# Performance work log

Measured on AMD Instinct MI355X. Metric: run time of the kernel, lower is better.

## Reference

```python
import jax, jax.numpy as jnp
import numpy as np

B, T, D, H, L = 2, 1000, 768, 12, 2
DK = D // H
MLP_HID = D * 1  # mlp_ratio = 1
WIDTHS = [7, 15, 31, 63, 127, 255, 7, 15, 31, 63, 127, 255]


def _band_mask():
    # diagonal_mask(seq_len, mask_width): True = blocked (outside the diagonal band)
    i = np.arange(T)[:, None]
    j = np.arange(T)[None, :]
    m = np.stack([np.abs(i - j) > (w // 2) for w in WIDTHS], 0)  # (H, T, T)
    return jnp.asarray(m)


def _rel_pos_emb():
    # espnet-style RelPositionalEncoding: rel positions T-1 .. -(T-1), shape (2T-1, D)
    pos = jnp.arange(T - 1, -T, -1, dtype=jnp.float32)
    div = jnp.exp(jnp.arange(0, D, 2, dtype=jnp.float32) * (-np.log(10000.0) / D))
    ang = pos[:, None] * div[None, :]
    return jnp.stack([jnp.sin(ang), jnp.cos(ang)], -1).reshape(2 * T - 1, D)


def setup_inputs() -> dict:
    key = jax.random.key(0)
    ks = iter(jax.random.split(key, 32))
    rn = lambda sh, s=0.02: jax.random.normal(next(ks), sh, jnp.float32) * s
    return {
        "x": jax.random.normal(next(ks), (B, T, D), jnp.float32),
        "mask": _band_mask(),
        "ln1_g": jnp.ones((L, D)), "ln1_b": jnp.zeros((L, D)),
        "wq": rn((L, D, D)), "bq": jnp.zeros((L, D)),
        "wk": rn((L, D, D)), "bk": jnp.zeros((L, D)),
        "wv": rn((L, D, D)), "bv": jnp.zeros((L, D)),
        "wo": rn((L, D, D)), "bo": jnp.zeros((L, D)),
        "wpos": rn((L, D, D)),
        "pbu": rn((L, H, DK)), "pbv": rn((L, H, DK)),
        "ln2_g": jnp.ones((L, D)), "ln2_b": jnp.zeros((L, D)),
        "w1": rn((L, D, MLP_HID)), "b1": jnp.zeros((L, MLP_HID)),
        "w2": rn((L, MLP_HID, D)), "b2": jnp.zeros((L, D)),
    }


def _ln(x, g, b):
    m = jnp.mean(x, -1, keepdims=True)
    v = jnp.var(x, -1, keepdims=True)
    return (x - m) * jax.lax.rsqrt(v + 1e-5) * g + b


def _rel_shift(x):
    # x: (b, h, t, 2t-1) -> shifted so column s corresponds to rel pos (t-1 - s + row offset)
    b, h, t, n = x.shape
    x = jnp.pad(x, ((0, 0), (0, 0), (0, 0), (1, 0)))        # (b,h,t,2t)
    x = x.reshape(b, h, n + 1, t)[:, :, 1:, :].reshape(b, h, t, n)
    return x[..., :t]


def _forward(x, mask, p):
    (ln1_g, ln1_b, wq, bq, wk, bk, wv, bv, wo, bo,
     wpos, pbu, pbv, ln2_g, ln2_b, w1, b1, w2, b2) = p
    pe = _rel_pos_emb()                                      # (2T-1, D)
    x = x * jnp.asarray(np.sqrt(D), x.dtype)                 # xscale in RelPositionalEncoding
    neg = jnp.asarray(-1e30, x.dtype)
    inv_sqrt_dk = 1.0 / np.sqrt(DK)
    for l in range(L):
        h = _ln(x, ln1_g[l], ln1_b[l])
        q = (h @ wq[l] + bq[l]).reshape(B, T, H, DK)
        k = (h @ wk[l] + bk[l]).reshape(B, T, H, DK)
        v = (h @ wv[l] + bv[l]).reshape(B, T, H, DK)
        pp = (pe @ wpos[l]).reshape(2 * T - 1, H, DK)        # pos projection (no bias)
        ac = jnp.einsum('bthd,bshd->bhts', q + pbu[l], k)    # content term
        bd = _rel_shift(jnp.einsum('bthd,nhd->bhtn', q + pbv[l], pp))  # position term
        s = (ac + bd) * inv_sqrt_dk
        s = jnp.where(mask[None], neg, s)                    # per-head diagonal band mask
        a = jax.nn.softmax(s, axis=-1)
        o = jnp.einsum('bhts,bshd->bthd', a, v).reshape(B, T, D) @ wo[l] + bo[l]
        x = x + o
        h2 = _ln(x, ln2_g[l], ln2_b[l])
        x = x + (jax.nn.gelu(h2 @ w1[l] + b1[l], approximate=False) @ w2[l] + b2[l])
    return x


def reference(x, mask, ln1_g, ln1_b, wq, bq, wk, bk, wv, bv, wo, bo, wpos, pbu, pbv, ln2_g, ln2_b, w1, b1, w2, b2):
    return _forward(x, mask, (ln1_g, ln1_b, wq, bq, wk, bk, wv, bv, wo, bo,
                              wpos, pbu, pbv, ln2_g, ln2_b, w1, b1, w2, b2))
```

## Files before the change

### kernel.cpp

```cpp
#include <hip/hip_runtime.h>

#define TT 1000
#define BB 2
#define DD 768
#define HH 12
#define DK 64
#define LL 2
#define WELEM 589824
#define PEROWS 255
#define VTP 1312
#define PPL 195840

typedef __bf16 bf16x8 __attribute__((ext_vector_type(8)));
typedef float floatx4 __attribute__((ext_vector_type(4)));

__device__ __constant__ int HALFW[12] = {3,7,15,31,63,127,3,7,15,31,63,127};
__device__ __constant__ int HORD[12]  = {5,11,4,10,3,9,2,8,1,7,0,6};

__device__ __forceinline__ float b2f(unsigned short u){
    union { unsigned int i; float f; } x; x.i = ((unsigned int)u) << 16; return x.f;
}
__device__ __forceinline__ unsigned short f2b(float f){
    union { float f; unsigned int i; } x; x.f = f;
    unsigned int i = x.i;
    i += 0x7fffu + ((i >> 16) & 1u);
    return (unsigned short)(i >> 16);
}
__device__ __forceinline__ void gload16(const void* g, void* l){
    __builtin_amdgcn_global_load_lds(
        (const __attribute__((address_space(1))) void*)g,
        (__attribute__((address_space(3))) void*)l, 16, 0, 0);
}

__global__ __launch_bounds__(256)
void prep_kernel(const float* s0, const float* s1, const float* s2, const float* s3,
                 const float* s4, const float* s5, const float* s6,
                 unsigned short* __restrict__ dst,
                 const float* __restrict__ x, float* __restrict__ xc,
                 unsigned short* __restrict__ pe){
    int z = blockIdx.z;
    int tid = threadIdx.x;
    if (z < 14){
        const float* srcs[7] = {s0,s1,s2,s3,s4,s5,s6};
        const float* src = srcs[z % 7] + (size_t)(z / 7)*WELEM;
        unsigned short* d = dst + (size_t)z*WELEM;
        int k0 = blockIdx.x*64, n0 = blockIdx.y*64;
        __shared__ __align__(16) unsigned short tile[64][72];
        int r = tid >> 2, c = tid & 3;
        const float4* sp = (const float4*)(src + (size_t)(k0+r)*DD + n0 + c*16);
        float4 f0 = sp[0], f1 = sp[1], f2 = sp[2], f3 = sp[3];
        unsigned short u[16];
        u[0]=f2b(f0.x); u[1]=f2b(f0.y); u[2]=f2b(f0.z); u[3]=f2b(f0.w);
        u[4]=f2b(f1.x); u[5]=f2b(f1.y); u[6]=f2b(f1.z); u[7]=f2b(f1.w);
        u[8]=f2b(f2.x); u[9]=f2b(f2.y); u[10]=f2b(f2.z); u[11]=f2b(f2.w);
        u[12]=f2b(f3.x); u[13]=f2b(f3.y); u[14]=f2b(f3.z); u[15]=f2b(f3.w);
        *(int4*)&tile[r][c*16]   = *(int4*)&u[0];
        *(int4*)&tile[r][c*16+8] = *(int4*)&u[8];
        __syncthreads();
        unsigned short tmp[16];
        #pragma unroll
        for (int i=0;i<16;++i) tmp[i] = tile[c*16+i][r];
        int4* dp = (int4*)(d + (size_t)(n0+r)*DD + k0 + c*16);
        dp[0] = *(int4*)&tmp[0];
        dp[1] = *(int4*)&tmp[8];
    } else if (z == 14){
        int id = blockIdx.y*12 + blockIdx.x;
        for (int i = id*256 + tid; i < 384000; i += 36864){
            float4 v = ((const float4*)x)[i];
            v.x *= 27.712812921102035f; v.y *= 27.712812921102035f;
            v.z *= 27.712812921102035f; v.w *= 27.712812921102035f;
            ((float4*)xc)[i] = v;
        }
    } else {
        int bid = blockIdx.y*12 + blockIdx.x;
        #pragma unroll
        for (int rr = 0; rr < 2; ++rr){
            int row = bid*2 + rr;
            if (row < PEROWS){
                float pos = (float)(127 - row);
                int i = tid;
                float dv = expf((float)(2*i) * (-9.210340371976184f / 768.0f));
                float ang = pos * dv;
                pe[(size_t)row*DD + 2*i]   = f2b(sinf(ang));
                pe[(size_t)row*DD + 2*i+1] = f2b(cosf(ang));
                if (tid < 128){
                    int j = 256 + tid;
                    float dv2 = expf((float)(2*j) * (-9.210340371976184f / 768.0f));
                    float an2 = pos * dv2;
                    pe[(size_t)row*DD + 2*j]   = f2b(sinf(an2));
                    pe[(size_t)row*DD + 2*j+1] = f2b(cosf(an2));
                }
            }
        }
    }
}

__global__ __launch_bounds__(256)
void ln_kernel(const float* __restrict__ x, const float* __restrict__ g,
               const float* __restrict__ bb, unsigned short* __restrict__ out){
    int row = blockIdx.x;
    const float* xr = x + (size_t)row*DD;
    int tid = threadIdx.x;
    float v0 = xr[tid], v1 = xr[tid+256], v2 = xr[tid+512];
    float s = v0+v1+v2, ss = v0*v0+v1*v1+v2*v2;
    #pragma unroll
    for (int o=1;o<64;o<<=1){ s += __shfl_xor(s,o); ss += __shfl_xor(ss,o); }
    __shared__ float rs[4], rss[4];
    int wv = tid>>6, lane = tid&63;
    if (lane==0){ rs[wv]=s; rss[wv]=ss; }
    __syncthreads();
    s  = rs[0]+rs[1]+rs[2]+rs[3];
    ss = rss[0]+rss[1]+rss[2]+rss[3];
    float mean = s * (1.0f/768.0f);
    float var  = ss * (1.0f/768.0f) - mean*mean;
    float inv  = 1.0f / sqrtf(var + 1e-5f);
    unsigned short* orow = out + (size_t)row*DD;
    #pragma unroll
    for (int kk=0;kk<3;++kk){
        int i = tid + 256*kk;
        float v = (kk==0?v0:(kk==1?v1:v2));
        orow[i] = f2b((v - mean)*inv*g[i] + bb[i]);
    }
}

#define GEMM_GL64(A_, Bt_, n0_, M_)                                             \
    int tid = threadIdx.x;                                                      \
    int m0 = blockIdx.x*64;                                                     \
    int wv = tid>>6, lane = tid&63;                                             \
    int quad = lane>>4, l16 = lane&15;                                          \
    floatx4 acc[4];                                                             \
    _Pragma("unroll")                                                           \
    for (int ni=0;ni<4;++ni) acc[ni] = (floatx4){0.f,0.f,0.f,0.f};              \
    {                                                                           \
      int rl0 = wv*16 + (lane>>3);                                              \
      int rl1 = rl0 + 8;                                                        \
      int gc  = (lane&7) ^ (lane>>3);                                           \
      int ra0 = m0 + rl0; if (ra0 > (M_)-1) ra0 = (M_)-1;                       \
      int ra1 = m0 + rl1; if (ra1 > (M_)-1) ra1 = (M_)-1;                       \
      const char* gA0 = (const char*)(A_)  + (size_t)ra0*1536 + gc*16;          \
      const char* gA1 = (const char*)(A_)  + (size_t)ra1*1536 + gc*16;          \
      const char* gB0 = (const char*)(Bt_) + (size_t)((n0_)+rl0)*1536 + gc*16;  \
      const char* gB1 = (const char*)(Bt_) + (size_t)((n0_)+rl1)*1536 + gc*16;  \
      char* shB = (char*)sh;                                                    \
      int ld0 = (2*wv)*1024, ld1 = (2*wv+1)*1024;                               \
      int arow = (16*wv + l16)*64;                                              \
      int sw8  = l16 & 7;                                                       \
      int cq0 = (quad ^ sw8)*8;                                                 \
      int cq1 = ((4|quad) ^ sw8)*8;                                             \
      gload16(gA0, shB + ld0);                                                  \
      gload16(gA1, shB + ld1);                                                  \
      gload16(gB0, shB + 8192 + ld0);                                           \
      gload16(gB1, shB + 8192 + ld1);                                           \
      for (int s=0; s<12; ++s){                                                 \
        if (s < 11){                                                            \
          char* nb = shB + ((s+1)&1)*16384;                                     \
          int off = (s+1)*128;                                                  \
          gload16(gA0 + off, nb + ld0);                                         \
          gload16(gA1 + off, nb + ld1);                                         \
          gload16(gB0 + off, nb + 8192 + ld0);                                  \
          gload16(gB1 + off, nb + 8192 + ld1);                                  \
          asm volatile("s_waitcnt vmcnt(4)" ::: "memory");                      \
        } else {                                                                \
          asm volatile("s_waitcnt vmcnt(0)" ::: "memory");                      \
        }                                                                       \
        __builtin_amdgcn_s_barrier();                                           \
        __builtin_amdgcn_sched_barrier(0);                                      \
        const unsigned short* cA = sh + (s&1)*8192;                             \
        const unsigned short* cB = cA + 4096;                                   \
        _Pragma("unroll")                                                       \
        for (int kh=0; kh<2; ++kh){                                             \
          int cq = kh ? cq1 : cq0;                                              \
          bf16x8 af = *(const bf16x8*)&cA[arow + cq];                           \
          _Pragma("unroll")                                                     \
          for (int ni=0; ni<4; ++ni){                                           \
            bf16x8 bfv = *(const bf16x8*)&cB[ni*1024 + l16*64 + cq];            \
            acc[ni] = __builtin_amdgcn_mfma_f32_16x16x32_bf16(af, bfv, acc[ni], 0,0,0); \
          }                                                                     \
        }                                                                       \
        __builtin_amdgcn_sched_barrier(0);                                      \
        __builtin_amdgcn_s_barrier();                                           \
      }                                                                         \
    }

template<int MODE>
__global__ __launch_bounds__(256)
void gemm_kernel(const unsigned short* __restrict__ A, const unsigned short* __restrict__ Bt,
                 const float* __restrict__ bias, unsigned short* __restrict__ outb,
                 float* __restrict__ resid, int M){
    __shared__ __align__(16) unsigned short sh[16384];
    int n0 = blockIdx.y*64;
    GEMM_GL64(A, Bt, n0, M)
    float bfv_[4];
    #pragma unroll
    for (int ni=0;ni<4;++ni) bfv_[ni] = bias ? bias[n0 + 16*ni + l16] : 0.0f;
    #pragma unroll
    for (int rr=0;rr<4;++rr){
        int row = m0 + 16*wv + 4*quad + rr;
        if (row >= M) continue;
        #pragma unroll
        for (int ni=0;ni<4;++ni){
            int col = n0 + 16*ni + l16;
            float v = acc[ni][rr] + bfv_[ni];
            if (MODE == 1)      outb[(size_t)row*768 + col] = f2b(0.5f*v*(1.0f + erff(v*0.70710678118654752f)));
            else                resid[(size_t)row*768 + col] += v;
        }
    }
}

__global__ __launch_bounds__(256)
void gemm_pos_kernel(const unsigned short* __restrict__ A, const unsigned short* __restrict__ Bt,
                     unsigned short* __restrict__ outb){
    __shared__ __align__(16) unsigned short sh[16384];
    int n0 = blockIdx.y*64;
    int zz = blockIdx.z;
    const unsigned short* Bt_ = Bt + (size_t)zz*7*WELEM;
    unsigned short* outb_ = outb + (size_t)zz*PPL;
    GEMM_GL64(A, Bt_, n0, PEROWS)
    #pragma unroll
    for (int rr=0;rr<4;++rr){
        int row = m0 + 16*wv + 4*quad + rr;
        if (row >= PEROWS) continue;
        #pragma unroll
        for (int ni=0;ni<4;++ni){
            int col = n0 + 16*ni + l16;
            int h = col >> 6, d = col & 63;
            outb_[((size_t)h*PEROWS + row)*DK + d] = f2b(acc[ni][rr]);
        }
    }
}

__global__ __launch_bounds__(256)
void gemm_qkv_kernel(const unsigned short* __restrict__ A, const unsigned short* __restrict__ Bt,
                     const float* __restrict__ bq, const float* __restrict__ bk, const float* __restrict__ bv,
                     unsigned short* __restrict__ qout, unsigned short* __restrict__ kout,
                     unsigned short* __restrict__ vout){
    __shared__ __align__(16) unsigned short sh[16384];
    int n0 = blockIdx.y*64;
    GEMM_GL64(A, Bt, n0, 2000)
    int sec = blockIdx.y / 12;
    int col0 = n0 - sec*768;
    int h = col0 >> 6;
    const float* bias = (sec==0) ? bq : (sec==1) ? bk : bv;
    float bfv_[4];
    #pragma unroll
    for (int ni=0;ni<4;++ni) bfv_[ni] = bias[col0 + 16*ni + l16];
    if (sec != 2){
        unsigned short* outp = (sec==0) ? qout : kout;
        #pragma unroll
        for (int rr=0;rr<4;++rr){
            int row = m0 + 16*wv + 4*quad + rr;
            if (row >= 2000) continue;
            int b = row / TT, tl = row - b*TT;
            #pragma unroll
            for (int ni=0;ni<4;++ni){
                int d = 16*ni + l16;
                outp[(((size_t)(b*HH + h))*TT + tl)*DK + d] = f2b(acc[ni][rr] + bfv_[ni]);
            }
        }
    } else {
        #pragma unroll
        for (int rr=0;rr<4;++rr){
            int rt = 16*wv + 4*quad + rr;
            #pragma unroll
            for (int ni=0;ni<4;++ni)
                sh[rt*66 + 16*ni + l16] = f2b(acc[ni][rr] + bfv_[ni]);
        }
        __syncthreads();
        #pragma unroll
        for (int it=0; it<16; ++it){
            int idx = it*256 + tid;
            int d = idx >> 6, rt = idx & 63;
            int row = m0 + rt;
            if (row < 2000){
                int b = row / TT, tl = row - b*TT;
                vout[(((size_t)(b*HH + h))*DK + d)*VTP + tl + 128] = sh[rt*66 + d];
            }
        }
    }
}

__global__ __launch_bounds__(256)
void attn_kernel(const unsigned short* __restrict__ q, const unsigned short* __restrict__ k,
                 const unsigned short* __restrict__ vT, const unsigned short* __restrict__ pp,
                 const float* __restrict__ pbu, const float* __restrict__ pbv,
                 unsigned short* __restrict__ out){
    int b = blockIdx.y, h = HORD[blockIdx.z];
    int t0 = blockIdx.x * 16;
    int w2 = HALFW[h];
    int tid = threadIdx.x;
    int wv = tid >> 6, lane = tid & 63;
    int l16 = lane & 15, quad = lane >> 4;

    const unsigned short* qB = q  + ((size_t)(b*HH + h))*TT*DK;
    const unsigned short* kB = k  + ((size_t)(b*HH + h))*TT*DK;
    const unsigned short* vB = vT + ((size_t)(b*HH + h))*DK*VTP;
    const unsigned short* pB = pp + (size_t)h*PEROWS*DK;

    __shared__ __align__(16) float bd[16*260];
    __shared__ __align__(16) unsigned short pl[16*328];
    __shared__ float sms[4][16];

    int tq = t0 + l16; if (tq > TT-1) tq = TT-1;
    union { int4 i; unsigned short u[8]; } r0, r1;
    r0.i = *(const int4*)(qB + (size_t)tq*DK + quad*8);
    r1.i = *(const int4*)(qB + (size_t)tq*DK + 32 + quad*8);
    const float* pu = pbu + h*DK + quad*8;
    const float* pv = pbv + h*DK + quad*8;
    union { unsigned short u[8]; bf16x8 v; } qu0, qu1, qv0, qv1;
    #pragma unroll
    for (int i=0;i<8;++i){
        float a0 = b2f(r0.u[i]), a1 = b2f(r1.u[i]);
        qu0.u[i] = f2b(a0 + pu[i]);
        qu1.u[i] = f2b(a1 + pu[32+i]);
        qv0.u[i] = f2b(a0 + pv[i]);
        qv1.u[i] = f2b(a1 + pv[32+i]);
    }

    int Nn = 2*w2 + 1;
    int ntiles = (Nn + 15) >> 4;
    for (int ti = wv; ti < ntiles; ti += 4){
        int n = 127 - w2 + ti*16 + l16; if (n > PEROWS-1) n = PEROWS-1;
        const unsigned short* pr = pB + (size_t)n*DK + quad*8;
        bf16x8 pb0 = *(const bf16x8*)pr;
        bf16x8 pb1 = *(const bf16x8*)(pr + 32);
        floatx4 a = {0.f,0.f,0.f,0.f};
        a = __builtin_amdgcn_mfma_f32_16x16x32_bf16(qv0.v, pb0, a, 0,0,0);
        a = __builtin_amdgcn_mfma_f32_16x16x32_bf16(qv1.v, pb1, a, 0,0,0);
        #pragma unroll
        for (int r=0;r<4;++r) bd[(quad*4+r)*260 + ti*16 + l16] = a[r];
    }
    for (int i = tid; i < 16*328/4; i += 256)
        ((unsigned long long*)pl)[i] = 0ULL;
    __syncthreads();

    int Ns = 2*w2 + 16;
    int stiles = (Ns + 15) >> 4;
    int s_lo = t0 - w2;
    float scv[5][4];
    #pragma unroll
    for (int ii = 0; ii < 5; ++ii){
        int ti = wv + ii*4;
        if (ti < stiles){
            int s = s_lo + ti*16 + l16;
            int sc = s < 0 ? 0 : (s > TT-1 ? TT-1 : s);
            const unsigned short* kr = kB + (size_t)sc*DK + quad*8;
            bf16x8 kb0 = *(const bf16x8*)kr;
            bf16x8 kb1 = *(const bf16x8*)(kr + 32);
            floatx4 a = {0.f,0.f,0.f,0.f};
            a = __builtin_amdgcn_mfma_f32_16x16x32_bf16(qu0.v, kb0, a, 0,0,0);
            a = __builtin_amdgcn_mfma_f32_16x16x32_bf16(qu1.v, kb1, a, 0,0,0);
            #pragma unroll
            for (int r=0;r<4;++r){
                int row = quad*4 + r;
                int nrel = ti*16 + l16 - row;
                bool ok = (nrel >= 0) && (nrel <= 2*w2) && (s >= 0) && (s <= TT-1);
                int idx = row*260 + nrel;
                idx = idx < 0 ? 0 : (idx > 16*260-1 ? 16*260-1 : idx);
                float bdv = bd[idx];
                scv[ii][r] = ok ? (a[r] + bdv) * 0.125f : -1e30f;
            }
        } else {
            #pragma unroll
            for (int r=0;r<4;++r) scv[ii][r] = -1e30f;
        }
    }

    float sm[4] = {0.f,0.f,0.f,0.f};
    #pragma unroll
    for (int ii = 0; ii < 5; ++ii){
        int ti = wv + ii*4;
        if (ti < stiles){
            int pad_base = (t0 - w2) - ((t0 - w2) & ~31);
            #pragma unroll
            for (int r=0;r<4;++r){
                float e = __expf(scv[ii][r]);
                sm[r] += e;
                pl[(quad*4+r)*328 + pad_base + ti*16 + l16] = f2b(e);
            }
        }
    }
    #pragma unroll
    for (int off=1; off<16; off<<=1){
        #pragma unroll
        for (int r=0;r<4;++r) sm[r] += __shfl_xor(sm[r], off);
    }
    if (l16 == 0){
        #pragma unroll
        for (int r=0;r<4;++r) sms[wv][quad*4+r] = sm[r];
    }
    __syncthreads();

    int s_lo2 = t0 - w2;
    int s0a = s_lo2 & ~31;
    int pad_lo = s_lo2 - s0a;
    int ktiles = (pad_lo + Ns + 31) >> 5;

    floatx4 oacc = {0.f,0.f,0.f,0.f};
    for (int kt = 0; kt < ktiles; ++kt){
        bf16x8 pa = *(const bf16x8*)&pl[l16*328 + kt*32 + quad*8];
        int sidx = s0a + kt*32 + quad*8 + 128;
        bf16x8 vb = *(const bf16x8*)(vB + (size_t)(wv*16 + l16)*VTP + sidx);
        oacc = __builtin_amdgcn_mfma_f32_16x16x32_bf16(pa, vb, oacc, 0,0,0);
    }
    #pragma unroll
    for (int r=0;r<4;++r){
        int row = quad*4 + r;
        float sum = sms[0][row] + sms[1][row] + sms[2][row] + sms[3][row];
        float rinv = sum > 0.f ? 1.0f/sum : 0.0f;
        int t = t0 + row;
        if (t <= TT-1)
            out[(((size_t)(b*TT + t))*HH + h)*DK + wv*16 + l16] = f2b(oacc[r] * rinv);
    }
}

extern "C" void kernel_launch(void* const* d_in, const int* in_sizes, int n_in,
                              void* d_out, int out_size, void* d_ws, size_t ws_size,
                              hipStream_t stream){
    const float* x    = (const float*)d_in[0];
    const float* ln1g = (const float*)d_in[2];
    const float* ln1b = (const float*)d_in[3];
    const float* wq   = (const float*)d_in[4];
    const float* bq   = (const float*)d_in[5];
    const float* wk   = (const float*)d_in[6];
    const float* bk   = (const float*)d_in[7];
    const float* wvv  = (const float*)d_in[8];
    const float* bv   = (const float*)d_in[9];
    const float* wo   = (const float*)d_in[10];
    const float* bo   = (const float*)d_in[11];
    const float* wpos = (const float*)d_in[12];
    const float* pbu  = (const float*)d_in[13];
    const float* pbv  = (const float*)d_in[14];
    const float* ln2g = (const float*)d_in[15];
    const float* ln2b = (const float*)d_in[16];
    const float* w1   = (const float*)d_in[17];
    const float* b1   = (const float*)d_in[18];
    const float* w2   = (const float*)d_in[19];
    const float* b2   = (const float*)d_in[20];

    const int NTOK = BB*TT;

    float* x_cur = (float*)d_out;

    char* ws = (char*)d_ws;
    unsigned short* qbuf  = (unsigned short*)(ws);
    unsigned short* kbuf  = (unsigned short*)(ws + 3072000);
    unsigned short* vTbuf = (unsigned short*)(ws + 6144000);
    unsigned short* hbuf  = (unsigned short*)(ws + 10174464);
    unsigned short* ppbuf = (unsigned short*)(ws + 13246464);
    unsigned short* pebuf = (unsigned short*)(ws + 14029824);
    unsigned short* wtbuf = (unsigned short*)(ws + 14421504);
    #define WT(t_,l_) (wtbuf + (size_t)((l_)*7 + (t_))*WELEM)

    dim3 blk(256);
    prep_kernel<<<dim3(12,12,16), blk, 0, stream>>>(wq, wk, wvv, wo, wpos, w1, w2,
                                                    wtbuf, x, x_cur, pebuf);
    gemm_pos_kernel<<<dim3(4,12,2), blk, 0, stream>>>(pebuf, WT(4,0), ppbuf);

    dim3 gBig(32, 12);
    dim3 gQKV(32, 36);
    dim3 gAttn(63, BB, HH);

    for (int l = 0; l < LL; ++l){
        long dl = (long)l*DD;
        long pl_ = (long)l*HH*DK;

        ln_kernel<<<NTOK, blk, 0, stream>>>(x_cur, ln1g + dl, ln1b + dl, hbuf);
        gemm_qkv_kernel<<<gQKV, blk, 0, stream>>>(hbuf, WT(0,l), bq + dl, bk + dl, bv + dl,
                                                  qbuf, kbuf, vTbuf);

        attn_kernel<<<gAttn, blk, 0, stream>>>(qbuf, kbuf, vTbuf, ppbuf + (size_t)l*PPL,
                                               pbu + pl_, pbv + pl_, hbuf);

        gemm_kernel<2><<<gBig, blk, 0, stream>>>(hbuf, WT(3,l), bo + dl, nullptr, x_cur, NTOK);

        ln_kernel<<<NTOK, blk, 0, stream>>>(x_cur, ln2g + dl, ln2b + dl, hbuf);
        gemm_kernel<1><<<gBig, blk, 0, stream>>>(hbuf, WT(5,l), b1 + dl, qbuf, nullptr, NTOK);
        gemm_kernel<2><<<gBig, blk, 0, stream>>>(qbuf, WT(6,l), b2 + dl, nullptr, x_cur, NTOK);
    }
}
```

Measured before the change: 282.7 us.

## Triple-buffer LDS in GEMM main loop to overlap loads with one barrier

Adds a three-stage LDS pipeline for the 64x64 GEMM tile used by the generic and positional GEMM kernels. Global loads run two k-steps ahead, and only one barrier per step is needed instead of a trailing barrier. The cost is 48KB of shared memory per block instead of 32KB, which may lower occupancy. The QKV GEMM still uses the old double-buffered macro.

```diff
diff --git a/kernel.cpp b/kernel.cpp
--- a/kernel.cpp
+++ b/kernel.cpp
@@ -182,14 +182,76 @@
       }                                                                         \
     }
 
+#define GEMM_GL64_3B(A_, Bt_, n0_, M_)                                          \
+    int tid = threadIdx.x;                                                      \
+    int m0 = blockIdx.x*64;                                                     \
+    int wv = tid>>6, lane = tid&63;                                             \
+    int quad = lane>>4, l16 = lane&15;                                          \
+    floatx4 acc[4];                                                             \
+    _Pragma("unroll")                                                           \
+    for (int ni=0;ni<4;++ni) acc[ni] = (floatx4){0.f,0.f,0.f,0.f};              \
+    {                                                                           \
+      int rl0 = wv*16 + (lane>>3);                                              \
+      int rl1 = rl0 + 8;                                                        \
+      int gc  = (lane&7) ^ (lane>>3);                                           \
+      int ra0 = m0 + rl0; if (ra0 > (M_)-1) ra0 = (M_)-1;                       \
+      int ra1 = m0 + rl1; if (ra1 > (M_)-1) ra1 = (M_)-1;                       \
+      const char* gA0 = (const char*)(A_)  + (size_t)ra0*1536 + gc*16;          \
+      const char* gA1 = (const char*)(A_)  + (size_t)ra1*1536 + gc*16;          \
+      const char* gB0 = (const char*)(Bt_) + (size_t)((n0_)+rl0)*1536 + gc*16;  \
+      const char* gB1 = (const char*)(Bt_) + (size_t)((n0_)+rl1)*1536 + gc*16;  \
+      char* shB = (char*)sh;                                                    \
+      int ld0 = (2*wv)*1024, ld1 = (2*wv+1)*1024;                               \
+      int arow = (16*wv + l16)*64;                                              \
+      int sw8  = l16 & 7;                                                       \
+      int cq0 = (quad ^ sw8)*8;                                                 \
+      int cq1 = ((4|quad) ^ sw8)*8;                                             \
+      gload16(gA0, shB + ld0);                                                  \
+      gload16(gA1, shB + ld1);                                                  \
+      gload16(gB0, shB + 8192 + ld0);                                           \
+      gload16(gB1, shB + 8192 + ld1);                                           \
+      gload16(gA0 + 128, shB + 16384 + ld0);                                    \
+      gload16(gA1 + 128, shB + 16384 + ld1);                                    \
+      gload16(gB0 + 128, shB + 16384 + 8192 + ld0);                             \
+      gload16(gB1 + 128, shB + 16384 + 8192 + ld1);                             \
+      for (int s=0; s<12; ++s){                                                 \
+        if (s < 11) asm volatile("s_waitcnt vmcnt(4)" ::: "memory");            \
+        else        asm volatile("s_waitcnt vmcnt(0)" ::: "memory");            \
+        __builtin_amdgcn_s_barrier();                                           \
+        __builtin_amdgcn_sched_barrier(0);                                      \
+        if (s < 10){                                                            \
+          char* nb = shB + ((s+2)%3)*16384;                                     \
+          int off = (s+2)*128;                                                  \
+          gload16(gA0 + off, nb + ld0);                                         \
+          gload16(gA1 + off, nb + ld1);                                         \
+          gload16(gB0 + off, nb + 8192 + ld0);                                  \
+          gload16(gB1 + off, nb + 8192 + ld1);                                  \
+        }                                                                       \
+        __builtin_amdgcn_sched_barrier(0);                                      \
+        const unsigned short* cA = sh + (s%3)*8192;                             \
+        const unsigned short* cB = cA + 4096;                                   \
+        _Pragma("unroll")                                                       \
+        for (int kh=0; kh<2; ++kh){                                             \
+          int cq = kh ? cq1 : cq0;                                              \
+          bf16x8 af = *(const bf16x8*)&cA[arow + cq];                           \
+          _Pragma("unroll")                                                     \
+          for (int ni=0; ni<4; ++ni){                                           \
+            bf16x8 bfv = *(const bf16x8*)&cB[ni*1024 + l16*64 + cq];            \
+            acc[ni] = __builtin_amdgcn_mfma_f32_16x16x32_bf16(af, bfv, acc[ni], 0,0,0); \
+          }                                                                     \
+        }                                                                       \
+        __builtin_amdgcn_sched_barrier(0);                                      \
+      }                                                                         \
+    }
+
 template<int MODE>
 __global__ __launch_bounds__(256)
 void gemm_kernel(const unsigned short* __restrict__ A, const unsigned short* __restrict__ Bt,
                  const float* __restrict__ bias, unsigned short* __restrict__ outb,
                  float* __restrict__ resid, int M){
-    __shared__ __align__(16) unsigned short sh[16384];
+    __shared__ __align__(16) unsigned short sh[24576];
     int n0 = blockIdx.y*64;
-    GEMM_GL64(A, Bt, n0, M)
+    GEMM_GL64_3B(A, Bt, n0, M)
     float bfv_[4];
     #pragma unroll
     for (int ni=0;ni<4;++ni) bfv_[ni] = bias ? bias[n0 + 16*ni + l16] : 0.0f;
@@ -210,12 +272,12 @@
 __global__ __launch_bounds__(256)
 void gemm_pos_kernel(const unsigned short* __restrict__ A, const unsigned short* __restrict__ Bt,
                      unsigned short* __restrict__ outb){
-    __shared__ __align__(16) unsigned short sh[16384];
+    __shared__ __align__(16) unsigned short sh[24576];
     int n0 = blockIdx.y*64;
     int zz = blockIdx.z;
     const unsigned short* Bt_ = Bt + (size_t)zz*7*WELEM;
     unsigned short* outb_ = outb + (size_t)zz*PPL;
-    GEMM_GL64(A, Bt_, n0, PEROWS)
+    GEMM_GL64_3B(A, Bt_, n0, PEROWS)
     #pragma unroll
     for (int rr=0;rr<4;++rr){
         int row = m0 + 16*wv + 4*quad + rr;
```

Measured after the change: 282.6 us. No clear change (-0.0%).
